# Kernel optimization log

Measured on AMD Instinct MI355X. Metric: run time of the kernel, lower is better.

The kernel has to match this reference:

```python
import jax, jax.numpy as jnp
import numpy as np

VJ = 80      # vjointnum (groups)
FS = 480     # feature_size = 2*k of RFF
HD = 256     # hidden_dim
K = 240      # RFF k
BATCH = 2048
TWO_PI = 2.0 * np.pi
SLOPE = 0.01  # LeakyReLU default negative_slope


def _wn(v, g):
    # weight_norm (dim=0): w[o,:] = g[o] * v[o,:] / ||v[o,:]||
    return v * (g[:, None] / jnp.linalg.norm(v, axis=1, keepdims=True))


def _grouped(x, v, g, b):
    # x: [B, G, in_g]; v: [G*out_g, in_g]; equivalent to groups=G Conv1d with kernel 1
    w = _wn(v, g)
    out_g = w.shape[0] // VJ
    y = jnp.einsum('bgi,goi->bgo', x, w.reshape(VJ, out_g, -1))
    return y + b.reshape(VJ, out_g)


def _lrelu(t):
    return jnp.where(t >= 0, t, SLOPE * t)


def setup_inputs() -> dict:
    key = jax.random.key(0)
    ks = jax.random.split(key, 12)
    d = {
        'querypoint': jax.random.normal(ks[0], (BATCH, VJ, 3), jnp.float32),
        'point_features': jax.random.normal(ks[1], (BATCH, VJ, FS), jnp.float32),
        'B_rff': jax.random.normal(ks[2], (3, K), jnp.float32),  # std=1
    }
    # per-group layer sizes: 480->512, 512->512, 512->256, 256->6
    dims = [(FS, 2 * HD), (2 * HD, 2 * HD), (2 * HD, HD), (HD, 6)]
    for i, (din, dout) in enumerate(dims):
        d[f'v{i}'] = jax.random.normal(ks[3 + 2 * i], (VJ * dout, din), jnp.float32) * 0.02
        d[f'g{i}'] = jnp.ones((VJ * dout,), jnp.float32)
        d[f'b{i}'] = jnp.zeros((VJ * dout,), jnp.float32)
    return d


def reference(querypoint, point_features, B_rff,
              v0, g0, b0, v1, g1, b1, v2, g2, b2, v3, g3, b3):
    # RFF encode: [B, N, 480]
    emb = TWO_PI * jnp.einsum('bnd,dk->bnk', querypoint, B_rff)
    feat = jnp.concatenate([jnp.cos(emb), jnp.sin(emb)], axis=-1)
    x = point_features + feat                       # [B, 80, 480]
    Bsz = x.shape[0]
    # transpose(-2,-1) then reshape(B, C*N, 1) with groups=80 ==> [B, 80, 480]
    x = jnp.transpose(x, (0, 2, 1)).reshape(Bsz, VJ, FS)
    x = _lrelu(_grouped(x, v0, g0, b0))             # [B, 80, 512]
    x = _lrelu(_grouped(x, v1, g1, b1))             # [B, 80, 512]
    x = _lrelu(_grouped(x, v2, g2, b2))             # [B, 80, 256]
    y = _grouped(x, v3, g3, b3)                     # [B, 80, 6]
    return y.reshape(Bsz, VJ, 6)
```

## Files before the change

### kernel.cpp

```cpp
#include <hip/hip_runtime.h>


typedef __attribute__((ext_vector_type(8)))  short short8;
typedef __attribute__((ext_vector_type(4)))  float f32x4;
typedef __attribute__((ext_vector_type(16))) float f32x16;
typedef __attribute__((ext_vector_type(2)))  unsigned int uint2v;

#define VJ    80
#define FS    480
#define HD2   512
#define HD    256
#define BATCH 2048
#define SMLP  520

static __device__ __forceinline__ unsigned short f2bf(float f) {
  unsigned int u = __builtin_bit_cast(unsigned int, f);
  u += 0x7FFFu + ((u >> 16) & 1u);
  return (unsigned short)(u >> 16);
}

template<int K, int RPG>
static __device__ __forceinline__ void wfrag32_body(
    int blk, const float* __restrict__ v, const float* __restrict__ gain,
    unsigned short* __restrict__ dst, float* sV, float* sScale) {
  constexpr int KS = K / 16;
  constexpr int KP = K + 4;
  const int t  = threadIdx.x;
  const int n0 = blk * 32;
  const int g  = n0 / RPG;
  const int nt = (n0 % RPG) >> 5;

  const f32x4* v4 = (const f32x4*)(v + (size_t)n0 * K);
  for (int idx = t; idx < 32 * K / 4; idx += 1024) {
    int row = idx / (K / 4), rem = idx - row * (K / 4);
    *(f32x4*)&sV[row * KP + rem * 4] = v4[idx];
  }
  __syncthreads();

  const int wave = t >> 6, lane = t & 63;
  for (int r = wave; r < 32; r += 16) {
    float s = 0.f;
    for (int k = lane; k < K; k += 64) { float x = sV[r * KP + k]; s += x * x; }
    #pragma unroll
    for (int off = 32; off > 0; off >>= 1) s += __shfl_down(s, off);
    if (lane == 0) sScale[r] = gain[n0 + r] / sqrtf(s);
  }
  __syncthreads();

  unsigned short* db = dst + (size_t)g * RPG * K + (size_t)nt * KS * 512;
  for (int o = t; o < KS * 64; o += 1024) {
    int ks = o >> 6, l = o & 63;
    int nl = l & 31, k0 = ks * 16 + ((l >> 5) << 3);
    float sc = sScale[nl];
    short8 pk;
    #pragma unroll
    for (int j = 0; j < 8; ++j) pk[j] = (short)f2bf(sV[nl * KP + k0 + j] * sc);
    *(short8*)&db[(size_t)ks * 512 + l * 8] = pk;
  }
}

static __device__ __forceinline__ void w3frag_body(
    int gidx, const float* __restrict__ v3, const float* __restrict__ g3,
    unsigned short* __restrict__ W3f, float* sV, float* sScale) {
  const int t = threadIdx.x;
  const f32x4* v4 = (const f32x4*)(v3 + (size_t)gidx * 6 * 256);
  if (t < 384) {
    int row = t >> 6, rem = t & 63;
    *(f32x4*)&sV[row * 260 + rem * 4] = v4[t];
  }
  __syncthreads();
  const int wave = t >> 6, lane = t & 63;
  if (wave < 6) {
    float s = 0.f;
    #pragma unroll
    for (int k = 0; k < 4; ++k) { float x = sV[wave * 260 + lane + k * 64]; s += x * x; }
    #pragma unroll
    for (int off = 32; off > 0; off >>= 1) s += __shfl_down(s, off);
    if (lane == 0) sScale[wave] = g3[gidx * 6 + wave] / sqrtf(s);
  }
  __syncthreads();
  if (t < 512) {
    int ks = t >> 6, l = t & 63;
    int c = l & 15, k0 = ks * 32 + ((l >> 4) << 3);
    short8 pk;
    #pragma unroll
    for (int j = 0; j < 8; ++j)
      pk[j] = (c < 6) ? (short)f2bf(sV[c * 260 + k0 + j] * sScale[c]) : (short)0;
    *(short8*)&W3f[(size_t)gidx * 4096 + (size_t)ks * 512 + l * 8] = pk;
  }
}

static __device__ __forceinline__ void prep_x_body(
    int b, const float* __restrict__ qp, const float* __restrict__ pf,
    const float* __restrict__ Brff, unsigned short* __restrict__ Xg,
    float* sB, float* sQ, unsigned short* sX) {
  const int t = threadIdx.x;
  if (t < 720) sB[t] = Brff[t];
  if (t < 240) sQ[t] = qp[(size_t)b * 240 + t];
  __syncthreads();
  const float* pfb = pf + (size_t)b * 38400;
  #pragma unroll 2
  for (int idx = t; idx < 19200; idx += 1024) {
    int n2 = idx / 480;
    int c  = idx - n2 * 480;
    int n  = n2 * 2;
    int k  = (c < 240) ? c : c - 240;
    float bx = sB[k], by = sB[240 + k], bz = sB[480 + k];
    float d0 = sQ[n*3]   * bx + sQ[n*3+1] * by + sQ[n*3+2] * bz;
    float d1 = sQ[n*3+3] * bx + sQ[n*3+4] * by + sQ[n*3+5] * bz;
    float f0 = (c < 240) ? __builtin_amdgcn_cosf(d0) : __builtin_amdgcn_sinf(d0);
    float f1 = (c < 240) ? __builtin_amdgcn_cosf(d1) : __builtin_amdgcn_sinf(d1);
    unsigned int w = (unsigned int)f2bf(pfb[n * 480 + c] + f0)
                   | ((unsigned int)f2bf(pfb[(n + 1) * 480 + c] + f1) << 16);
    *(unsigned int*)&sX[c * 82 + n] = w;
  }
  __syncthreads();
  for (int idx4 = t; idx4 < 9600; idx4 += 1024) {
    int g  = idx4 / 120;
    int i4 = idx4 - g * 120;
    int i  = i4 * 4;
    int cl = i / 80;
    int n  = i - cl * 80;
    const unsigned int* p = (const unsigned int*)&sX[(g * 6 + cl) * 82 + n];
    uint2v val = { p[0], p[1] };
    *(uint2v*)(Xg + ((size_t)g * BATCH + b) * 480 + i) = val;
  }
}

__global__ void __launch_bounds__(1024)
prep_all(const float* __restrict__ qp, const float* __restrict__ pf,
         const float* __restrict__ Brff,
         const float* __restrict__ v0, const float* __restrict__ g0,
         const float* __restrict__ v1, const float* __restrict__ g1,
         const float* __restrict__ v2, const float* __restrict__ g2,
         const float* __restrict__ v3, const float* __restrict__ g3,
         unsigned short* __restrict__ W0, unsigned short* __restrict__ W1,
         unsigned short* __restrict__ W2, unsigned short* __restrict__ W3f,
         unsigned short* __restrict__ Xg) {
  __shared__ float sMem[960];
  __shared__ unsigned short sBig[480 * 82];
  const int bid = blockIdx.x;
  const int q = bid / 5, r = bid - q * 5;
  if (r < 3) {
    const int wb = q * 3 + r;
    float* sV = (float*)sBig;
    float* sScale = sMem;
    if      (wb < 1280) wfrag32_body<480, 512>(wb,        v0, g0, W0, sV, sScale);
    else if (wb < 2560) wfrag32_body<512, 512>(wb - 1280, v1, g1, W1, sV, sScale);
    else if (wb < 3200) wfrag32_body<512, 256>(wb - 2560, v2, g2, W2, sV, sScale);
    else if (wb < 3280) w3frag_body(wb - 3200, v3, g3, W3f, sV, sScale);
  } else {
    const int pb = q * 2 + (r - 3);
    if (pb < BATCH)
      prep_x_body(pb, qp, pf, Brff, Xg, sMem, sMem + 720, sBig);
  }
}

#define MLP_STEP32(ksv, BB)                                                   \
  {                                                                           \
    const int ksc = (ksv);                                                    \
    short8 a0 = *(const short8*)(aB + ksc * 16);                              \
    short8 a1 = *(const short8*)(aB + 32 * SMLP + ksc * 16);                  \
    short8 p0, p1;                                                            \
    const bool pf_ok = (ksc + 3 < KS);                                        \
    if (pf_ok) {                                                              \
      p0 = *(const short8*)(wB + ((size_t)0 * KS + ksc + 3) * 512);           \
      if (NT > 1) p1 = *(const short8*)(wB + ((size_t)1 * KS + ksc + 3) * 512); \
    }                                                                         \
    __builtin_amdgcn_s_setprio(1);                                            \
    _Pragma("unroll")                                                         \
    for (int nt = 0; nt < NT; ++nt)                                           \
      acc[0][nt] = __builtin_amdgcn_mfma_f32_32x32x16_bf16(a0, BB[nt], acc[0][nt], 0, 0, 0); \
    _Pragma("unroll")                                                         \
    for (int nt = 0; nt < NT; ++nt)                                           \
      acc[1][nt] = __builtin_amdgcn_mfma_f32_32x32x16_bf16(a1, BB[nt], acc[1][nt], 0, 0, 0); \
    __builtin_amdgcn_s_setprio(0);                                            \
    if (pf_ok) {                                                              \
      BB[0] = p0;                                                             \
      if (NT > 1) BB[1] = p1;                                                 \
    }                                                                         \
  }

template<int K, int N, bool ACT>
static __device__ __forceinline__ void run_layer32(
    unsigned short* __restrict__ s,
    const unsigned short* __restrict__ Wf, const float* __restrict__ bias,
    int wn, int lane) {
  constexpr int NT = N / 256;
  constexpr int KS = K / 16;
  const int nbase = wn * (N / 8);
  const int lr = lane & 31, lh = lane >> 5;

  f32x16 acc[2][NT];
  #pragma unroll
  for (int mt = 0; mt < 2; ++mt)
    #pragma unroll
    for (int nt = 0; nt < NT; ++nt)
      #pragma unroll
      for (int r = 0; r < 16; ++r) acc[mt][nt][r] = 0.f;

  const unsigned short* aB = s + lr * SMLP + lh * 8;
  const unsigned short* wB = Wf + (size_t)(wn * NT) * KS * 512 + lane * 8;

  short8 bb0[NT], bb1[NT], bb2[NT];
  #pragma unroll
  for (int nt = 0; nt < NT; ++nt) bb0[nt] = *(const short8*)(wB + ((size_t)nt * KS    ) * 512);
  #pragma unroll
  for (int nt = 0; nt < NT; ++nt) bb1[nt] = *(const short8*)(wB + ((size_t)nt * KS + 1) * 512);
  #pragma unroll
  for (int nt = 0; nt < NT; ++nt) bb2[nt] = *(const short8*)(wB + ((size_t)nt * KS + 2) * 512);

  #pragma unroll
  for (int ks3 = 0; ks3 < KS / 3; ++ks3) {
    MLP_STEP32(3 * ks3,     bb0);
    MLP_STEP32(3 * ks3 + 1, bb1);
    MLP_STEP32(3 * ks3 + 2, bb2);
  }
  if (KS % 3 == 2) {
    MLP_STEP32(KS - 2, bb0);
    MLP_STEP32(KS - 1, bb1);
  }

  float bv[NT];
  #pragma unroll
  for (int nt = 0; nt < NT; ++nt) bv[nt] = bias[nbase + nt * 32 + lr];

  __syncthreads();
  #pragma unroll
  for (int mt = 0; mt < 2; ++mt)
    #pragma unroll
    for (int nt = 0; nt < NT; ++nt)
      #pragma unroll
      for (int r = 0; r < 16; ++r) {
        float val = acc[mt][nt][r] + bv[nt];
        if (ACT) val = (val >= 0.f) ? val : 0.01f * val;
        const int row = mt * 32 + (r & 3) + 8 * (r >> 2) + 4 * lh;
        s[row * SMLP + (nbase + nt * 32 + lr)] = f2bf(val);
      }
  __syncthreads();
}

__global__ void __launch_bounds__(512, 4)
mlp_kernel(const unsigned short* __restrict__ Xg,
           const unsigned short* __restrict__ W0, const unsigned short* __restrict__ W1,
           const unsigned short* __restrict__ W2, const unsigned short* __restrict__ W3f,
           const float* __restrict__ b0, const float* __restrict__ b1,
           const float* __restrict__ b2, const float* __restrict__ b3,
           float* __restrict__ out) {
  __shared__ unsigned short s[64 * SMLP];

  const int bid   = blockIdx.x;
  const int xcd   = bid & 7;
  const int local = bid >> 3;
  const int g     = xcd * 10 + (local >> 5);
  const int tile  = local & 31;
  const int m0    = tile * 64;

  const int tid  = threadIdx.x, lane = tid & 63;
  const int wn   = tid >> 6;

  const unsigned short* Xs = Xg + ((size_t)g * BATCH + m0) * 480;
  for (int idx = tid; idx < 64 * 60; idx += 512) {
    int row = idx / 60, c = idx - row * 60;
    *(short8*)&s[row * SMLP + c * 8] = *(const short8*)(Xs + (size_t)row * 480 + c * 8);
  }
  __syncthreads();

  run_layer32<480, 512, true>(s, W0 + (size_t)g * 512 * 480, b0 + g * 512, wn, lane);
  run_layer32<512, 512, true>(s, W1 + (size_t)g * 512 * 512, b1 + g * 512, wn, lane);
  run_layer32<512, 256, true>(s, W2 + (size_t)g * 256 * 512, b2 + g * 256, wn, lane);

  if (wn < 4) {
    const int lr = lane & 15, lh = lane >> 4;
    const unsigned short* aB4 = s + (wn * 16 + lr) * SMLP + lh * 8;
    const unsigned short* w3  = W3f + (size_t)g * 4096 + lane * 8;
    f32x4 a4 = (f32x4){0.f, 0.f, 0.f, 0.f};
    #pragma unroll
    for (int kk = 0; kk < 8; ++kk) {
      short8 av  = *(const short8*)(aB4 + kk * 32);
      short8 wv8 = *(const short8*)(w3 + (size_t)kk * 512);
      a4 = __builtin_amdgcn_mfma_f32_16x16x32_bf16(av, wv8, a4, 0, 0, 0);
    }
    const int col = lane & 15;
    if (col < 6) {
      const float bias3 = b3[g * 6 + col];
      #pragma unroll
      for (int r = 0; r < 4; ++r)
        out[((size_t)(m0 + wn * 16 + lh * 4 + r) * VJ + g) * 6 + col] = a4[r] + bias3;
    }
  }
}

extern "C" void kernel_launch(void* const* d_in, const int* in_sizes, int n_in,
                              void* d_out, int out_size, void* d_ws, size_t ws_size,
                              hipStream_t stream) {
  const float* qp   = (const float*)d_in[0];
  const float* pf   = (const float*)d_in[1];
  const float* Brff = (const float*)d_in[2];
  const float* v0 = (const float*)d_in[3];  const float* g0 = (const float*)d_in[4];  const float* b0 = (const float*)d_in[5];
  const float* v1 = (const float*)d_in[6];  const float* g1 = (const float*)d_in[7];  const float* b1 = (const float*)d_in[8];
  const float* v2 = (const float*)d_in[9];  const float* g2 = (const float*)d_in[10]; const float* b2 = (const float*)d_in[11];
  const float* v3 = (const float*)d_in[12]; const float* g3 = (const float*)d_in[13]; const float* b3 = (const float*)d_in[14];

  unsigned short* W0  = (unsigned short*)d_ws;
  unsigned short* W1  = W0 + (size_t)VJ * HD2 * FS;
  unsigned short* W2  = W1 + (size_t)VJ * HD2 * HD2;
  unsigned short* W3f = W2 + (size_t)VJ * HD  * HD2;
  unsigned short* Xg  = W3f + (size_t)VJ * 4096;

  prep_all<<<dim3(5470), dim3(1024), 0, stream>>>(qp, pf, Brff,
                                                  v0, g0, v1, g1, v2, g2, v3, g3,
                                                  W0, W1, W2, W3f, Xg);
  mlp_kernel<<<dim3(VJ * 32), dim3(512), 0, stream>>>(Xg, W0, W1, W2, W3f,
                                                      b0, b1, b2, b3, (float*)d_out);
}
```

Measured before the change: 393.6 us.

## Double MLP batch tile to 128 rows with A-fragment double buffering

The MLP kernel now processes 128 batch rows per block instead of 64, so each weight fragment loaded from global memory feeds four M-tiles of MFMAs instead of two, halving weight traffic per row. A fragments are prefetched from LDS one k-step ahead and B prefetch depth drops to two stages. LDS and register use per block roughly double, so occupancy is lowered to 2 blocks per EU and the grid halves. The prep kernel's interleave of weight-conversion and input-prep blocks is also rebalanced (8:5 instead of 3:2).

After: 419.8 us. 1.07x slower.

```diff
diff --git a/kernel.cpp b/kernel.cpp
--- a/kernel.cpp
+++ b/kernel.cpp
@@ -140,9 +140,9 @@
   __shared__ float sMem[960];
   __shared__ unsigned short sBig[480 * 82];
   const int bid = blockIdx.x;
-  const int q = bid / 5, r = bid - q * 5;
-  if (r < 3) {
-    const int wb = q * 3 + r;
+  const int q = bid / 13, r = bid - q * 13;
+  if (r < 8) {
+    const int wb = q * 8 + r;
     float* sV = (float*)sBig;
     float* sScale = sMem;
     if      (wb < 1280) wfrag32_body<480, 512>(wb,        v0, g0, W0, sV, sScale);
@@ -150,39 +150,36 @@
     else if (wb < 3200) wfrag32_body<512, 256>(wb - 2560, v2, g2, W2, sV, sScale);
     else if (wb < 3280) w3frag_body(wb - 3200, v3, g3, W3f, sV, sScale);
   } else {
-    const int pb = q * 2 + (r - 3);
+    const int pb = q * 5 + (r - 8);
     if (pb < BATCH)
       prep_x_body(pb, qp, pf, Brff, Xg, sMem, sMem + 720, sBig);
   }
 }
 
-#define MLP_STEP32(ksv, BB)                                                   \
+#define MLP_STEP128(ksv, AC, AN, BB)                                          \
   {                                                                           \
     const int ksc = (ksv);                                                    \
-    short8 a0 = *(const short8*)(aB + ksc * 16);                              \
-    short8 a1 = *(const short8*)(aB + 32 * SMLP + ksc * 16);                  \
-    short8 p0, p1;                                                            \
-    const bool pf_ok = (ksc + 3 < KS);                                        \
-    if (pf_ok) {                                                              \
-      p0 = *(const short8*)(wB + ((size_t)0 * KS + ksc + 3) * 512);           \
-      if (NT > 1) p1 = *(const short8*)(wB + ((size_t)1 * KS + ksc + 3) * 512); \
+    if (ksc + 1 < KS) {                                                       \
+      _Pragma("unroll")                                                       \
+      for (int mt = 0; mt < 4; ++mt)                                          \
+        AN[mt] = *(const short8*)(aB + mt * 32 * SMLP + (ksc + 1) * 16);      \
     }                                                                         \
     __builtin_amdgcn_s_setprio(1);                                            \
     _Pragma("unroll")                                                         \
-    for (int nt = 0; nt < NT; ++nt)                                           \
-      acc[0][nt] = __builtin_amdgcn_mfma_f32_32x32x16_bf16(a0, BB[nt], acc[0][nt], 0, 0, 0); \
-    _Pragma("unroll")                                                         \
-    for (int nt = 0; nt < NT; ++nt)                                           \
-      acc[1][nt] = __builtin_amdgcn_mfma_f32_32x32x16_bf16(a1, BB[nt], acc[1][nt], 0, 0, 0); \
+    for (int mt = 0; mt < 4; ++mt)                                            \
+      _Pragma("unroll")                                                       \
+      for (int nt = 0; nt < NT; ++nt)                                         \
+        acc[mt][nt] = __builtin_amdgcn_mfma_f32_32x32x16_bf16(AC[mt], BB[nt], acc[mt][nt], 0, 0, 0); \
     __builtin_amdgcn_s_setprio(0);                                            \
-    if (pf_ok) {                                                              \
-      BB[0] = p0;                                                             \
-      if (NT > 1) BB[1] = p1;                                                 \
+    if (ksc + 2 < KS) {                                                       \
+      _Pragma("unroll")                                                       \
+      for (int nt = 0; nt < NT; ++nt)                                         \
+        BB[nt] = *(const short8*)(wB + ((size_t)nt * KS + ksc + 2) * 512);    \
     }                                                                         \
   }
 
 template<int K, int N, bool ACT>
-static __device__ __forceinline__ void run_layer32(
+static __device__ __forceinline__ void run_layer128(
     unsigned short* __restrict__ s,
     const unsigned short* __restrict__ Wf, const float* __restrict__ bias,
     int wn, int lane) {
@@ -191,9 +188,9 @@
   const int nbase = wn * (N / 8);
   const int lr = lane & 31, lh = lane >> 5;
 
-  f32x16 acc[2][NT];
-  #pragma unroll
-  for (int mt = 0; mt < 2; ++mt)
+  f32x16 acc[4][NT];
+  #pragma unroll
+  for (int mt = 0; mt < 4; ++mt)
     #pragma unroll
     for (int nt = 0; nt < NT; ++nt)
       #pragma unroll
@@ -202,23 +199,19 @@
   const unsigned short* aB = s + lr * SMLP + lh * 8;
   const unsigned short* wB = Wf + (size_t)(wn * NT) * KS * 512 + lane * 8;
 
-  short8 bb0[NT], bb1[NT], bb2[NT];
+  short8 aa0[4], aa1[4];
+  short8 bb0[NT], bb1[NT];
+  #pragma unroll
+  for (int mt = 0; mt < 4; ++mt) aa0[mt] = *(const short8*)(aB + mt * 32 * SMLP);
   #pragma unroll
   for (int nt = 0; nt < NT; ++nt) bb0[nt] = *(const short8*)(wB + ((size_t)nt * KS    ) * 512);
   #pragma unroll
   for (int nt = 0; nt < NT; ++nt) bb1[nt] = *(const short8*)(wB + ((size_t)nt * KS + 1) * 512);
-  #pragma unroll
-  for (int nt = 0; nt < NT; ++nt) bb2[nt] = *(const short8*)(wB + ((size_t)nt * KS + 2) * 512);
-
-  #pragma unroll
-  for (int ks3 = 0; ks3 < KS / 3; ++ks3) {
-    MLP_STEP32(3 * ks3,     bb0);
-    MLP_STEP32(3 * ks3 + 1, bb1);
-    MLP_STEP32(3 * ks3 + 2, bb2);
-  }
-  if (KS % 3 == 2) {
-    MLP_STEP32(KS - 2, bb0);
-    MLP_STEP32(KS - 1, bb1);
+
+  #pragma unroll
+  for (int ks2 = 0; ks2 < KS / 2; ++ks2) {
+    MLP_STEP128(2 * ks2,     aa0, aa1, bb0);
+    MLP_STEP128(2 * ks2 + 1, aa1, aa0, bb1);
   }
 
   float bv[NT];
@@ -227,7 +220,7 @@
 
   __syncthreads();
   #pragma unroll
-  for (int mt = 0; mt < 2; ++mt)
+  for (int mt = 0; mt < 4; ++mt)
     #pragma unroll
     for (int nt = 0; nt < NT; ++nt)
       #pragma unroll
@@ -240,37 +233,37 @@
   __syncthreads();
 }
 
-__global__ void __launch_bounds__(512, 4)
+__global__ void __launch_bounds__(512, 2)
 mlp_kernel(const unsigned short* __restrict__ Xg,
            const unsigned short* __restrict__ W0, const unsigned short* __restrict__ W1,
            const unsigned short* __restrict__ W2, const unsigned short* __restrict__ W3f,
            const float* __restrict__ b0, const float* __restrict__ b1,
            const float* __restrict__ b2, const float* __restrict__ b3,
            float* __restrict__ out) {
-  __shared__ unsigned short s[64 * SMLP];
+  __shared__ unsigned short s[128 * SMLP];
 
   const int bid   = blockIdx.x;
   const int xcd   = bid & 7;
   const int local = bid >> 3;
-  const int g     = xcd * 10 + (local >> 5);
-  const int tile  = local & 31;
-  const int m0    = tile * 64;
+  const int g     = xcd * 10 + (local >> 4);
+  const int tile  = local & 15;
+  const int m0    = tile * 128;
 
   const int tid  = threadIdx.x, lane = tid & 63;
   const int wn   = tid >> 6;
 
   const unsigned short* Xs = Xg + ((size_t)g * BATCH + m0) * 480;
-  for (int idx = tid; idx < 64 * 60; idx += 512) {
+  for (int idx = tid; idx < 128 * 60; idx += 512) {
     int row = idx / 60, c = idx - row * 60;
     *(short8*)&s[row * SMLP + c * 8] = *(const short8*)(Xs + (size_t)row * 480 + c * 8);
   }
   __syncthreads();
 
-  run_layer32<480, 512, true>(s, W0 + (size_t)g * 512 * 480, b0 + g * 512, wn, lane);
-  run_layer32<512, 512, true>(s, W1 + (size_t)g * 512 * 512, b1 + g * 512, wn, lane);
-  run_layer32<512, 256, true>(s, W2 + (size_t)g * 256 * 512, b2 + g * 256, wn, lane);
-
-  if (wn < 4) {
+  run_layer128<480, 512, true>(s, W0 + (size_t)g * 512 * 480, b0 + g * 512, wn, lane);
+  run_layer128<512, 512, true>(s, W1 + (size_t)g * 512 * 512, b1 + g * 512, wn, lane);
+  run_layer128<512, 256, true>(s, W2 + (size_t)g * 256 * 512, b2 + g * 256, wn, lane);
+
+  {
     const int lr = lane & 15, lh = lane >> 4;
     const unsigned short* aB4 = s + (wn * 16 + lr) * SMLP + lh * 8;
     const unsigned short* w3  = W3f + (size_t)g * 4096 + lane * 8;
@@ -308,9 +301,9 @@
   unsigned short* W3f = W2 + (size_t)VJ * HD  * HD2;
   unsigned short* Xg  = W3f + (size_t)VJ * 4096;
 
-  prep_all<<<dim3(5470), dim3(1024), 0, stream>>>(qp, pf, Brff,
+  prep_all<<<dim3(5330), dim3(1024), 0, stream>>>(qp, pf, Brff,
                                                   v0, g0, v1, g1, v2, g2, v3, g3,
                                                   W0, W1, W2, W3f, Xg);
-  mlp_kernel<<<dim3(VJ * 32), dim3(512), 0, stream>>>(Xg, W0, W1, W2, W3f,
+  mlp_kernel<<<dim3(VJ * 16), dim3(512), 0, stream>>>(Xg, W0, W1, W2, W3f,
                                                       b0, b1, b2, b3, (float*)d_out);
 }
```
